# Optimization experiments

Hardware: AMD Instinct MI355X
Metric: run time of the kernel (lower is better)

Reference implementation:

```python
import jax, jax.numpy as jnp
import numpy as np

B, N1, N2, D, K = 8, 2048, 512, 128, 32
LEVELS, RES, BASE, FC = 3, 3, 0.25, 192
R3 = RES ** 3  # 27 voxel bins per level
EPS = 1e-5


def group_norm(x, gamma, beta, groups):
    # x: [b, C, ...]; normalize per (group) over channel-subset + spatial dims
    b, c = x.shape[0], x.shape[1]
    xg = x.reshape(b, groups, -1)
    mu = xg.mean(axis=-1, keepdims=True)
    var = xg.var(axis=-1, keepdims=True)
    xn = ((xg - mu) * jax.lax.rsqrt(var + EPS)).reshape(x.shape)
    shape = (1, c) + (1,) * (x.ndim - 2)
    return xn * gamma.reshape(shape) + beta.reshape(shape)


def prelu(x, a):
    return jnp.where(x >= 0, x, a * x)


def setup_inputs() -> dict:
    key = jax.random.key(0)
    ks = jax.random.split(key, 12)
    def w(k, shape):
        fan_in = shape[-1]
        return jax.random.uniform(k, shape, jnp.float32, -1.0, 1.0) / jnp.sqrt(jnp.float32(fan_in))
    return {
        "coords": jax.random.normal(ks[0], (B, N1, 3), jnp.float32),
        "coords2": jax.random.normal(ks[1], (B, N2, 3), jnp.float32),
        "fmap1": jax.random.normal(ks[2], (B, D, N1), jnp.float32),
        "fmap2": jax.random.normal(ks[3], (B, D, N2), jnp.float32),
        # vol_conv: Conv1d(81,128,1) -> GN(8,128) -> PReLU -> Conv1d(128,192,1)
        "W1": w(ks[4], (128, R3 * LEVELS)), "b1": jnp.zeros((128,), jnp.float32),
        "g1": jnp.ones((128,), jnp.float32), "be1": jnp.zeros((128,), jnp.float32),
        "a1": jnp.array(0.25, jnp.float32),
        "W2": w(ks[5], (FC, 128)), "b2": jnp.zeros((FC,), jnp.float32),
        # knn_conv: Conv2d(4,64,1) -> GN(8,64) -> PReLU;  knn_out: Conv1d(64,192,1)
        "Wk": w(ks[6], (64, 4)), "bk": jnp.zeros((64,), jnp.float32),
        "gk": jnp.ones((64,), jnp.float32), "bek": jnp.zeros((64,), jnp.float32),
        "ak": jnp.array(0.25, jnp.float32),
        "Wo": w(ks[7], (FC, 64)), "bo": jnp.zeros((FC,), jnp.float32),
    }


def reference(coords, coords2, fmap1, fmap2, W1, b1, g1, be1, a1, W2, b2,
              Wk, bk, gk, bek, ak, Wo, bo):
    b, n1 = coords.shape[0], coords.shape[1]
    n2 = coords2.shape[1]
    dim = fmap1.shape[1]

    # correlation: [b, n1, n2]
    corr = jnp.einsum('bdn,bdm->bnm', fmap1, fmap2) / jnp.sqrt(jnp.float32(dim))
    # pairwise offsets template - search: [b, n1, n2, 3]
    diff = coords2[:, None, :, :] - coords[:, :, None, :]

    # --- multi-level voxel feature via scatter-add ---
    base = jnp.arange(b * n1, dtype=jnp.int32).reshape(b, n1, 1) * R3
    feats = []
    for i in range(LEVELS):
        r = BASE * (2 ** i)
        dv = jnp.round(diff / r)
        valid = jnp.all(jnp.abs(dv) <= (RES // 2), axis=-1)          # [b,n1,n2]
        dvi = (dv + 1.0).astype(jnp.int32)
        cube = dvi[..., 0] * (RES * RES) + dvi[..., 1] * RES + dvi[..., 2]
        idx = jnp.where(valid, cube, 0)                              # torch: cube*valid
        seg = (base + idx).reshape(-1)
        vf = valid.astype(corr.dtype)
        nseg = b * n1 * R3
        add = jax.ops.segment_sum((corr * vf).reshape(-1), seg, num_segments=nseg).reshape(b, n1, R3)
        cnt = jax.ops.segment_sum(vf.reshape(-1), seg, num_segments=nseg).reshape(b, n1, R3)
        feats.append((add / jnp.clip(cnt, 1.0, float(n1))).transpose(0, 2, 1))  # [b,R3,n1]
    vol = jnp.concatenate(feats, axis=1)                             # [b, 3*27, n1]

    h = jnp.einsum('oc,bcn->bon', W1, vol) + b1[None, :, None]
    h = prelu(group_norm(h, g1, be1, 8), a1)
    vol_out = jnp.einsum('oc,bcn->bon', W2, h) + b2[None, :, None]   # [b, FC, n1]

    # --- KNN feature ---
    dist = jnp.sum(diff * diff, axis=-1)                             # [b,n1,n2]
    _, nbr = jax.lax.top_k(-dist, K)                                 # [b,n1,K]
    knn_corr = jnp.take_along_axis(corr, nbr, axis=2)                # [b,n1,K]
    knn_xyz = jnp.take_along_axis(diff, nbr[..., None], axis=2)      # [b,n1,K,3]
    e = jnp.concatenate([knn_corr[:, None], knn_xyz.transpose(0, 3, 1, 2)], axis=1)  # [b,4,n1,K]
    h = jnp.einsum('oc,bcnk->bonk', Wk, e) + bk[None, :, None, None]
    h = prelu(group_norm(h, gk, bek, 8), ak)
    h = jnp.max(h, axis=3)                                           # [b,64,n1]
    knn_out = jnp.einsum('oc,bcn->bon', Wo, h) + bo[None, :, None]   # [b,FC,n1]

    return vol_out + knn_out
```

## Files before the change

kernel.cpp:

```cpp
#include <hip/hip_runtime.h>
#include <hip/hip_bf16.h>

#define N1 2048
#define N2 512
#define KNN 32

typedef unsigned short u16;
typedef unsigned int u32;
typedef unsigned long long u64;
typedef __attribute__((ext_vector_type(8))) short bf16x8;
typedef __attribute__((ext_vector_type(4))) float f32x4;

#define OFF_W1B  18432
#define OFF_GV   36864
#define OFF_GK   36992
#define OFF_FLAG 37120
#define OFF_H1   37128
#define OFF_KM   1085704
#define OFF_CO   1609992

__device__ __forceinline__ float tof(u16 u) {
  union { u32 i; float f; } v; v.i = ((u32)u) << 16; return v.f;
}
__device__ __forceinline__ u16 tob(float f) {
  __hip_bfloat16 h = __float2bfloat16(f);
  return *reinterpret_cast<u16*>(&h);
}
__device__ __forceinline__ float fs(float v) {
  return (fabsf(v) < 1e30f) ? v : 0.f;
}

template <int BF>
__device__ __forceinline__ float LD(const void* p, size_t i) {
  if (BF) return tof(((const u16*)p)[i]);
  return ((const float*)p)[i];
}
template <int BF>
__device__ __forceinline__ void ST(void* p, size_t i, float v) {
  if (BF) ((u16*)p)[i] = tob(v);
  else    ((float*)p)[i] = v;
}

__device__ __forceinline__ u32 umin32(u32 a, u32 b) { return a < b ? a : b; }

__device__ __forceinline__ u32 wave_min_u32(u32 v) {
  v = umin32(v, (u32)__builtin_amdgcn_update_dpp((int)0xFFFFFFFF, (int)v, 0x111, 0xf, 0xf, false));
  v = umin32(v, (u32)__builtin_amdgcn_update_dpp((int)0xFFFFFFFF, (int)v, 0x112, 0xf, 0xf, false));
  v = umin32(v, (u32)__builtin_amdgcn_update_dpp((int)0xFFFFFFFF, (int)v, 0x114, 0xf, 0xf, false));
  v = umin32(v, (u32)__builtin_amdgcn_update_dpp((int)0xFFFFFFFF, (int)v, 0x118, 0xf, 0xf, false));
  v = umin32(v, (u32)__builtin_amdgcn_update_dpp((int)0xFFFFFFFF, (int)v, 0x142, 0xa, 0xf, false));
  v = umin32(v, (u32)__builtin_amdgcn_update_dpp((int)0xFFFFFFFF, (int)v, 0x143, 0xc, 0xf, false));
  return (u32)__builtin_amdgcn_readlane((int)v, 63);
}

template <int BF>
__device__ __forceinline__ bf16x8 ld_wfrag(const void* W2, const void* Wo,
                                           int o, int k0) {
  if (BF) {
    const u16* p = (k0 < 128) ? (const u16*)W2 + (size_t)o * 128 + k0
                              : (const u16*)Wo + (size_t)o * 64 + (k0 - 128);
    return *(const bf16x8*)p;
  } else {
    const float* p = (k0 < 128) ? (const float*)W2 + (size_t)o * 128 + k0
                                : (const float*)Wo + (size_t)o * 64 + (k0 - 128);
    bf16x8 r;
#pragma unroll
    for (int j = 0; j < 8; j++) r[j] = (short)tob(p[j]);
    return r;
  }
}

template <int BF>
__device__ void prep_body(const void* W1, float* ws, int i0, int stride) {
  u16* w1b = (u16*)(ws + OFF_W1B);
  for (int i = i0; i < 128 * 96; i += stride) {
    int c = i / 96, j = i % 96;
    float v = (j < 81) ? LD<BF>(W1, c * 81 + j) : 0.f;
    w1b[i] = tob(fs(v));
  }
}

__global__ __launch_bounds__(256) void k_prep(const void* fmap1, const void* W1,
                                              float* ws) {
  int t = threadIdx.x;
  __shared__ int sbad;
  if (t == 0) sbad = 0;
  __syncthreads();
  int bad = 0;
  const u16* fm = (const u16*)fmap1;
  for (int i = t * 8; i < t * 8 + 8; i++) {
    float v = tof(fm[i]);
    if (!(fabsf(v) <= 64.f)) bad = 1;
  }
  if (bad) atomicOr(&sbad, 1);
  __syncthreads();
  int bf = sbad ? 0 : 1;
  if (blockIdx.x == 0) {
    if (t == 0) ((int*)(ws + OFF_FLAG))[0] = bf;
    (ws + OFF_GV)[t] = 0.f;
  }
  int i0 = blockIdx.x * 256 + t, stride = gridDim.x * 256;
  if (bf) prep_body<1>(W1, ws, i0, stride);
  else    prep_body<0>(W1, ws, i0, stride);
}

template <int BF>
__device__ void corr_stage(const void* f1, const void* f2, u16* As, u16* Bs,
                           int b, int m0, int n0, int t) {
#pragma unroll
  for (int rep = 0; rep < 2; rep++) {
    int i = t + rep * 256;
    int m8 = i & 15, d4 = i >> 4;
    u16 e[4][8];
    if (BF) {
      const u16* F1 = (const u16*)f1;
#pragma unroll
      for (int dr = 0; dr < 4; dr++) {
        uint4 v = *(const uint4*)&F1[(size_t)(b * 128 + d4 * 4 + dr) * N1 + m0 + m8 * 8];
        u32 w[4] = {v.x, v.y, v.z, v.w};
#pragma unroll
        for (int j = 0; j < 8; j++) e[dr][j] = (u16)(w[j >> 1] >> ((j & 1) * 16));
      }
    } else {
      const float* F1 = (const float*)f1;
#pragma unroll
      for (int dr = 0; dr < 4; dr++) {
        const float* src = &F1[(size_t)(b * 128 + d4 * 4 + dr) * N1 + m0 + m8 * 8];
        float4 a = *(const float4*)src, c = *(const float4*)(src + 4);
        float f[8] = {a.x, a.y, a.z, a.w, c.x, c.y, c.z, c.w};
#pragma unroll
        for (int j = 0; j < 8; j++) e[dr][j] = tob(f[j]);
      }
    }
#pragma unroll
    for (int j = 0; j < 8; j++) {
      u64 pk = (u64)e[0][j] | ((u64)e[1][j] << 16) | ((u64)e[2][j] << 32) |
               ((u64)e[3][j] << 48);
      *(u64*)&As[(m8 * 8 + j) * 136 + d4 * 4] = pk;
    }
  }
  {
    int n8 = t & 7, d4 = t >> 3;
    u16 e[4][8];
    if (BF) {
      const u16* F2 = (const u16*)f2;
#pragma unroll
      for (int dr = 0; dr < 4; dr++) {
        uint4 v = *(const uint4*)&F2[(size_t)(b * 128 + d4 * 4 + dr) * N2 + n0 + n8 * 8];
        u32 w[4] = {v.x, v.y, v.z, v.w};
#pragma unroll
        for (int j = 0; j < 8; j++) e[dr][j] = (u16)(w[j >> 1] >> ((j & 1) * 16));
      }
    } else {
      const float* F2 = (const float*)f2;
#pragma unroll
      for (int dr = 0; dr < 4; dr++) {
        const float* src = &F2[(size_t)(b * 128 + d4 * 4 + dr) * N2 + n0 + n8 * 8];
        float4 a = *(const float4*)src, c = *(const float4*)(src + 4);
        float f[8] = {a.x, a.y, a.z, a.w, c.x, c.y, c.z, c.w};
#pragma unroll
        for (int j = 0; j < 8; j++) e[dr][j] = tob(f[j]);
      }
    }
#pragma unroll
    for (int j = 0; j < 8; j++) {
      u64 pk = (u64)e[0][j] | ((u64)e[1][j] << 16) | ((u64)e[2][j] << 32) |
               ((u64)e[3][j] << 48);
      *(u64*)&Bs[(n8 * 8 + j) * 136 + d4 * 4] = pk;
    }
  }
}

__global__ __launch_bounds__(256) void k_corr(const int* flag,
                                              const void* f1, const void* f2,
                                              u16* corrb) {
  __shared__ __attribute__((aligned(16))) u16 As[128 * 136];
  __shared__ __attribute__((aligned(16))) u16 Bs[64 * 136];
  int b = blockIdx.z, m0 = blockIdx.x * 128, n0 = blockIdx.y * 64, t = threadIdx.x;
  if (*flag) corr_stage<1>(f1, f2, As, Bs, b, m0, n0, t);
  else       corr_stage<0>(f1, f2, As, Bs, b, m0, n0, t);
  __syncthreads();

  int wv = t >> 6, lane = t & 63;
  int l15 = lane & 15, q = lane >> 4;
  int wm = (wv >> 1) * 64, wn = (wv & 1) * 32;
  f32x4 acc[4][2];
#pragma unroll
  for (int mt = 0; mt < 4; mt++)
#pragma unroll
    for (int nt = 0; nt < 2; nt++) acc[mt][nt] = (f32x4){0.f, 0.f, 0.f, 0.f};

#pragma unroll
  for (int kc = 0; kc < 128; kc += 32) {
    bf16x8 af[4], bf[2];
#pragma unroll
    for (int mt = 0; mt < 4; mt++)
      af[mt] = *(const bf16x8*)&As[(wm + mt * 16 + l15) * 136 + kc + q * 8];
#pragma unroll
    for (int nt = 0; nt < 2; nt++)
      bf[nt] = *(const bf16x8*)&Bs[(wn + nt * 16 + l15) * 136 + kc + q * 8];
#pragma unroll
    for (int mt = 0; mt < 4; mt++)
#pragma unroll
      for (int nt = 0; nt < 2; nt++)
        acc[mt][nt] = __builtin_amdgcn_mfma_f32_16x16x32_bf16(
            af[mt], bf[nt], acc[mt][nt], 0, 0, 0);
  }
  const float s = 0.08838834764831843f;
#pragma unroll
  for (int mt = 0; mt < 4; mt++)
#pragma unroll
    for (int nt = 0; nt < 2; nt++)
#pragma unroll
      for (int r = 0; r < 4; r++) {
        int m = m0 + wm + mt * 16 + q * 4 + r;
        int n = n0 + wn + nt * 16 + l15;
        corrb[((size_t)(b * N1 + m)) * N2 + n] = tob(acc[mt][nt][r] * s);
      }
}

template <int BF>
__device__ void pv_body(const void* coords, const void* coords2,
                        const u16* corrb, const void* Wk, const void* bk,
                        const u16* w1b, const void* b1,
                        u16* h1b, u16* knnmax,
                        float* gvolraw, float* gknnraw,
                        float* c2s, float* binsum, float* bincnt,
                        float4* e_s, u16* volb, float* statv, float* statk,
                        int b, int p0, int t) {
  int wv = t >> 6, lane = t & 63;
  int l15 = lane & 15, q = lane >> 4;
  for (int i = t; i < N2 * 3; i += 256) c2s[i] = LD<BF>(coords2, b * N2 * 3 + i);
  for (int i = t; i < 208; i += 256) ((uint4*)volb)[i] = make_uint4(0, 0, 0, 0);
  if (t < 16) { statv[t] = 0.f; statk[t] = 0.f; }
  __syncthreads();

  for (int s = 0; s < 2; s++) {
    int pp = wv * 2 + s;
    int p = p0 + pp;
    for (int i = lane; i < 81; i += 64) {
      binsum[wv * 81 + i] = 0.f;
      bincnt[wv * 81 + i] = 0.f;
    }
    float px = LD<BF>(coords, (b * N1 + p) * 3 + 0);
    float py = LD<BF>(coords, (b * N1 + p) * 3 + 1);
    float pz = LD<BF>(coords, (b * N1 + p) * 3 + 2);
    const u16* crow = corrb + ((size_t)(b * N1 + p)) * N2;

    u64 kk[8];
#pragma unroll
    for (int i = 0; i < 8; i++) {
      int n2 = i * 64 + lane;
      float cv = tof(crow[n2]);
      float dx = c2s[n2 * 3 + 0] - px;
      float dy = c2s[n2 * 3 + 1] - py;
      float dz = c2s[n2 * 3 + 2] - pz;
      float dist = __fadd_rn(__fadd_rn(__fmul_rn(dx, dx), __fmul_rn(dy, dy)),
                             __fmul_rn(dz, dz));
      union { float f; u32 u; } du; du.f = dist;
      kk[i] = (((u64)du.u) << 32) | (u64)n2;
      float sc = 4.f;
#pragma unroll
      for (int lvl = 0; lvl < 3; lvl++) {
        float vx = rintf(dx * sc), vy = rintf(dy * sc), vz = rintf(dz * sc);
        if (fabsf(vx) <= 1.f && fabsf(vy) <= 1.f && fabsf(vz) <= 1.f) {
          int cube = ((int)vx + 1) * 9 + ((int)vy + 1) * 3 + ((int)vz + 1);
          atomicAdd(&binsum[wv * 81 + lvl * 27 + cube], cv);
          atomicAdd(&bincnt[wv * 81 + lvl * 27 + cube], 1.f);
        }
        sc *= 0.5f;
      }
    }

#define CAS(a, b) { u64 x = kk[a], y = kk[b]; bool sw = y < x; \
                    kk[a] = sw ? y : x; kk[b] = sw ? x : y; }
    CAS(0,1) CAS(2,3) CAS(4,5) CAS(6,7)
    CAS(0,2) CAS(1,3) CAS(4,6) CAS(5,7)
    CAS(1,2) CAS(5,6)
    CAS(0,4) CAS(1,5) CAS(2,6) CAS(3,7)
    CAS(2,4) CAS(3,5)
    CAS(1,2) CAS(3,4) CAS(5,6)
#undef CAS
    int my_idx = 0;
    for (int it = 0; it < KNN; it++) {
      u32 hb = (u32)(kk[0] >> 32);
      u32 wb = wave_min_u32(hb);
      u64 mask = __ballot(hb == wb);
      u32 widx;
      if (__builtin_popcountll(mask) == 1) {
        int wl = (int)__builtin_ctzll(mask);
        widx = (u32)__builtin_amdgcn_readlane((int)(u32)kk[0], wl);
      } else {
        u32 hidx = (hb == wb) ? (u32)kk[0] : 0xFFFFFFFFu;
        widx = wave_min_u32(hidx);
      }
      if (lane == it) my_idx = (int)widx;
      if (lane == (int)(widx & 63u)) {
        kk[0] = kk[1]; kk[1] = kk[2]; kk[2] = kk[3]; kk[3] = kk[4];
        kk[4] = kk[5]; kk[5] = kk[6]; kk[6] = kk[7]; kk[7] = ~0ull;
      }
    }
    if (lane < KNN) {
      float4 ev;
      ev.x = tof(crow[my_idx]);
      ev.y = c2s[my_idx * 3 + 0] - px;
      ev.z = c2s[my_idx * 3 + 1] - py;
      ev.w = c2s[my_idx * 3 + 2] - pz;
      e_s[wv * 32 + lane] = ev;
    }
#pragma unroll
    for (int rep = 0; rep < 2; rep++) {
      int i = lane + rep * 64;
      if (i < 96) {
        float v = (i < 81)
            ? binsum[wv * 81 + i] / fmaxf(bincnt[wv * 81 + i], 1.f) : 0.f;
        volb[pp * 104 + i] = tob(v);
      }
    }

    {
      int cch = lane;
      float w0 = LD<BF>(Wk, cch * 4 + 0), w1 = LD<BF>(Wk, cch * 4 + 1);
      float w2 = LD<BF>(Wk, cch * 4 + 2), w3 = LD<BF>(Wk, cch * 4 + 3);
      float bv = LD<BF>(bk, cch);
      float sm = 0.f, sq = 0.f, mx = -3e38f;
#pragma unroll 8
      for (int k = 0; k < KNN; k++) {
        float4 ev = e_s[wv * 32 + k];
        float h = bv + w0 * ev.x + w1 * ev.y + w2 * ev.z + w3 * ev.w;
        sm += h; sq += h * h; mx = fmaxf(mx, h);
      }
      knnmax[((size_t)(b * N1 + p)) * 64 + cch] = tob(mx);
      sm += __shfl_xor(sm, 1, 64); sq += __shfl_xor(sq, 1, 64);
      sm += __shfl_xor(sm, 2, 64); sq += __shfl_xor(sq, 2, 64);
      sm += __shfl_xor(sm, 4, 64); sq += __shfl_xor(sq, 4, 64);
      if ((lane & 7) == 0) {
        int g = cch >> 3;
        atomicAdd(&statk[g * 2 + 0], sm);
        atomicAdd(&statk[g * 2 + 1], sq);
      }
    }
  }
  __syncthreads();

  f32x4 acc[2];
  acc[0] = (f32x4){0.f, 0.f, 0.f, 0.f};
  acc[1] = (f32x4){0.f, 0.f, 0.f, 0.f};
#pragma unroll
  for (int kc = 0; kc < 96; kc += 32) {
    bf16x8 af = *(const bf16x8*)&volb[l15 * 104 + kc + q * 8];
    bf16x8 bf0 = *(const bf16x8*)&w1b[((2 * wv + 0) * 16 + l15) * 96 + kc + q * 8];
    bf16x8 bf1 = *(const bf16x8*)&w1b[((2 * wv + 1) * 16 + l15) * 96 + kc + q * 8];
    acc[0] = __builtin_amdgcn_mfma_f32_16x16x32_bf16(af, bf0, acc[0], 0, 0, 0);
    acc[1] = __builtin_amdgcn_mfma_f32_16x16x32_bf16(af, bf1, acc[1], 0, 0, 0);
  }
#pragma unroll
  for (int ct = 0; ct < 2; ct++) {
    int c = (2 * wv + ct) * 16 + l15;
    float bias = LD<BF>(b1, c);
    float sm = 0.f, sq = 0.f;
    if (q < 2) {
#pragma unroll
      for (int r = 0; r < 4; r++) {
        int p = p0 + q * 4 + r;
        float v = acc[ct][r] + bias;
        h1b[((size_t)(b * N1 + p)) * 128 + c] = tob(v);
        sm += v; sq += v * v;
      }
    }
    sm += __shfl_xor(sm, 1, 64);  sq += __shfl_xor(sq, 1, 64);
    sm += __shfl_xor(sm, 2, 64);  sq += __shfl_xor(sq, 2, 64);
    sm += __shfl_xor(sm, 4, 64);  sq += __shfl_xor(sq, 4, 64);
    sm += __shfl_xor(sm, 8, 64);  sq += __shfl_xor(sq, 8, 64);
    sm += __shfl_xor(sm, 16, 64); sq += __shfl_xor(sq, 16, 64);
    sm += __shfl_xor(sm, 32, 64); sq += __shfl_xor(sq, 32, 64);
    if (lane == 0) {
      int g = 2 * wv + ct;
      atomicAdd(&statv[g * 2 + 0], sm);
      atomicAdd(&statv[g * 2 + 1], sq);
    }
  }
  __syncthreads();
  if (t < 16) atomicAdd(&gvolraw[b * 16 + t], statv[t]);
  else if (t < 32) atomicAdd(&gknnraw[b * 16 + (t - 16)], statk[t - 16]);
}

__global__ __launch_bounds__(256) void k_pv(const int* flag,
                                            const void* coords, const void* coords2,
                                            const u16* corrb, const void* Wk,
                                            const void* bk, const u16* w1b,
                                            const void* b1, u16* h1b,
                                            u16* knnmax, float* gvolraw,
                                            float* gknnraw) {
  __shared__ float c2s[N2 * 3];
  __shared__ float binsum[4 * 81];
  __shared__ float bincnt[4 * 81];
  __shared__ float4 e_s[4 * 32];
  __shared__ __attribute__((aligned(16))) u16 volb[16 * 104];
  __shared__ float statv[16], statk[16];
  int b = blockIdx.y, p0 = blockIdx.x * 8, t = threadIdx.x;
  if (*flag)
    pv_body<1>(coords, coords2, corrb, Wk, bk, w1b, b1, h1b, knnmax,
               gvolraw, gknnraw, c2s, binsum, bincnt, e_s, volb, statv, statk,
               b, p0, t);
  else
    pv_body<0>(coords, coords2, corrb, Wk, bk, w1b, b1, h1b, knnmax,
               gvolraw, gknnraw, c2s, binsum, bincnt, e_s, volb, statv, statk,
               b, p0, t);
}

template <int BF>
__device__ void out_body(const u16* h1b, const u16* knnmax,
                         const void* W2, const void* Wo,
                         const float* gvolraw, const float* gknnraw,
                         const void* g1, const void* be1, const void* a1p,
                         const void* gk, const void* bek, const void* akp,
                         const void* b2, const void* bo, void* out,
                         float* Ac, float* Bc, float* Sc, float* Bi, u16* gs,
                         int b, int p0, int t) {
  if (t < 192) {
    float A, Bv, slope;
    if (t < 128) {
      int g = t >> 4;
      float S = fs(gvolraw[b * 16 + g * 2 + 0]);
      float Q = fs(gvolraw[b * 16 + g * 2 + 1]);
      float mean = S / 32768.f;
      float var = fmaxf(Q / 32768.f - mean * mean, 0.f);
      float inv = 1.f / sqrtf(var + 1e-5f);
      A = inv * LD<BF>(g1, t); Bv = LD<BF>(be1, t) - mean * A;
      slope = LD<BF>(a1p, 0);
    } else {
      int c = t - 128, g = c >> 3;
      float S = fs(gknnraw[b * 16 + g * 2 + 0]);
      float Q = fs(gknnraw[b * 16 + g * 2 + 1]);
      float mean = S / 524288.f;
      float var = fmaxf(Q / 524288.f - mean * mean, 0.f);
      float inv = 1.f / sqrtf(var + 1e-5f);
      A = inv * LD<BF>(gk, c); Bv = LD<BF>(bek, c) - mean * A;
      slope = LD<BF>(akp, 0);
    }
    Ac[t] = A; Bc[t] = Bv; Sc[t] = slope;
    Bi[t] = LD<BF>(b2, t) + LD<BF>(bo, t);
  }
  __syncthreads();

  for (int i = t; i < 768; i += 256) {
    int p = i / 24, c8 = i % 24;
    int c0 = c8 * 8;
    uint4 v;
    if (c8 < 16) v = *(const uint4*)&h1b[((size_t)(b * N1 + p0 + p)) * 128 + c0];
    else         v = *(const uint4*)&knnmax[((size_t)(b * N1 + p0 + p)) * 64 + (c0 - 128)];
    u16 e[8] = {(u16)(v.x & 0xffff), (u16)(v.x >> 16), (u16)(v.y & 0xffff),
                (u16)(v.y >> 16),    (u16)(v.z & 0xffff), (u16)(v.z >> 16),
                (u16)(v.w & 0xffff), (u16)(v.w >> 16)};
    u16 r[8];
#pragma unroll
    for (int j = 0; j < 8; j++) {
      int c = c0 + j;
      float xn = tof(e[j]) * Ac[c] + Bc[c];
      xn = xn >= 0.f ? xn : Sc[c] * xn;
      r[j] = tob(xn);
    }
    uint4 wv;
    wv.x = (u32)r[0] | ((u32)r[1] << 16);
    wv.y = (u32)r[2] | ((u32)r[3] << 16);
    wv.z = (u32)r[4] | ((u32)r[5] << 16);
    wv.w = (u32)r[6] | ((u32)r[7] << 16);
    *(uint4*)&gs[p * 200 + c0] = wv;
  }
  __syncthreads();

  int wv2 = t >> 6, lane = t & 63;
  int l15 = lane & 15, q = lane >> 4;
  int obase = wv2 * 48;
  f32x4 acc[3][2];
#pragma unroll
  for (int mt = 0; mt < 3; mt++)
#pragma unroll
    for (int nt = 0; nt < 2; nt++) acc[mt][nt] = (f32x4){0.f, 0.f, 0.f, 0.f};

#pragma unroll
  for (int kc = 0; kc < 192; kc += 32) {
    bf16x8 af[3], bf[2];
#pragma unroll
    for (int mt = 0; mt < 3; mt++)
      af[mt] = ld_wfrag<BF>(W2, Wo, obase + mt * 16 + l15, kc + q * 8);
#pragma unroll
    for (int nt = 0; nt < 2; nt++)
      bf[nt] = *(const bf16x8*)&gs[(nt * 16 + l15) * 200 + kc + q * 8];
#pragma unroll
    for (int mt = 0; mt < 3; mt++)
#pragma unroll
      for (int nt = 0; nt < 2; nt++)
        acc[mt][nt] = __builtin_amdgcn_mfma_f32_16x16x32_bf16(
            af[mt], bf[nt], acc[mt][nt], 0, 0, 0);
  }
#pragma unroll
  for (int mt = 0; mt < 3; mt++)
#pragma unroll
    for (int nt = 0; nt < 2; nt++)
#pragma unroll
      for (int r = 0; r < 4; r++) {
        int o = obase + mt * 16 + q * 4 + r;
        int p = p0 + nt * 16 + l15;
        ST<BF>(out, ((size_t)(b * 192 + o)) * N1 + p, fs(acc[mt][nt][r] + Bi[o]));
      }
}

__global__ __launch_bounds__(256) void k_out(const int* flag,
                                             const u16* h1b, const u16* knnmax,
                                             const void* W2, const void* Wo,
                                             const float* gvolraw, const float* gknnraw,
                                             const void* g1, const void* be1,
                                             const void* a1p, const void* gk,
                                             const void* bek, const void* akp,
                                             const void* b2, const void* bo,
                                             void* out) {
  __shared__ float Ac[192], Bc[192], Sc[192], Bi[192];
  __shared__ __attribute__((aligned(16))) u16 gs[32 * 200];
  int b = blockIdx.y, p0 = blockIdx.x * 32, t = threadIdx.x;
  if (*flag)
    out_body<1>(h1b, knnmax, W2, Wo, gvolraw, gknnraw, g1, be1, a1p, gk, bek,
                akp, b2, bo, out, Ac, Bc, Sc, Bi, gs, b, p0, t);
  else
    out_body<0>(h1b, knnmax, W2, Wo, gvolraw, gknnraw, g1, be1, a1p, gk, bek,
                akp, b2, bo, out, Ac, Bc, Sc, Bi, gs, b, p0, t);
}

extern "C" void kernel_launch(void* const* d_in, const int* in_sizes, int n_in,
                              void* d_out, int out_size, void* d_ws, size_t ws_size,
                              hipStream_t stream) {
  const void* coords  = d_in[0];
  const void* coords2 = d_in[1];
  const void* fmap1   = d_in[2];
  const void* fmap2   = d_in[3];
  const void* W1  = d_in[4];
  const void* b1  = d_in[5];
  const void* g1  = d_in[6];
  const void* be1 = d_in[7];
  const void* a1  = d_in[8];
  const void* W2  = d_in[9];
  const void* b2  = d_in[10];
  const void* Wk  = d_in[11];
  const void* bk  = d_in[12];
  const void* gk  = d_in[13];
  const void* bek = d_in[14];
  const void* ak  = d_in[15];
  const void* Wo  = d_in[16];
  const void* bo  = d_in[17];

  float* ws = (float*)d_ws;
  u16* w1b       = (u16*)(ws + OFF_W1B);
  float* gvolraw = ws + OFF_GV;
  float* gknnraw = ws + OFF_GK;
  const int* flag = (const int*)(ws + OFF_FLAG);
  u16* h1b    = (u16*)(ws + OFF_H1);
  u16* knnmax = (u16*)(ws + OFF_KM);
  u16* corrb  = (u16*)(ws + OFF_CO);

  k_prep<<<dim3(8), dim3(256), 0, stream>>>(fmap1, W1, ws);
  k_corr<<<dim3(16, 8, 8), dim3(256), 0, stream>>>(flag, fmap1, fmap2, corrb);
  k_pv<<<dim3(256, 8), dim3(256), 0, stream>>>(flag, coords, coords2, corrb,
                                               Wk, bk, w1b, b1, h1b, knnmax,
                                               gvolraw, gknnraw);
  k_out<<<dim3(64, 8), dim3(256), 0, stream>>>(flag, h1b, knnmax, W2, Wo,
                                               gvolraw, gknnraw, g1, be1, a1,
                                               gk, bek, ak, b2, bo, d_out);
}
```

Baseline: 208.2 us.

## Fold prep kernel into corr, detect dtype per block, and pair-process KNN points per wave

Removes the separate prep kernel: every block now re-detects the input dtype from fmap1 itself, and one corr block converts W1 and zeroes the stats buffer. In k_pv each wave now handles its two points at once, interleaving the distance, binning, top-k selection and the fused DPP min reduction so both chains share latency. This drops one launch and adds ILP in the serial selection loop, at the cost of more registers and doubled shared bin buffers. It also relies on the corr block finishing the W1 conversion before k_pv reads it, which holds under stream ordering.

Result: slower. 214.6 us (+3.1%).

```diff
diff --git a/kernel.cpp b/kernel.cpp
--- a/kernel.cpp
+++ b/kernel.cpp
@@ -14,7 +14,6 @@
 #define OFF_W1B  18432
 #define OFF_GV   36864
 #define OFF_GK   36992
-#define OFF_FLAG 37120
 #define OFF_H1   37128
 #define OFF_KM   1085704
 #define OFF_CO   1609992
@@ -43,14 +42,33 @@
 
 __device__ __forceinline__ u32 umin32(u32 a, u32 b) { return a < b ? a : b; }
 
-__device__ __forceinline__ u32 wave_min_u32(u32 v) {
-  v = umin32(v, (u32)__builtin_amdgcn_update_dpp((int)0xFFFFFFFF, (int)v, 0x111, 0xf, 0xf, false));
-  v = umin32(v, (u32)__builtin_amdgcn_update_dpp((int)0xFFFFFFFF, (int)v, 0x112, 0xf, 0xf, false));
-  v = umin32(v, (u32)__builtin_amdgcn_update_dpp((int)0xFFFFFFFF, (int)v, 0x114, 0xf, 0xf, false));
-  v = umin32(v, (u32)__builtin_amdgcn_update_dpp((int)0xFFFFFFFF, (int)v, 0x118, 0xf, 0xf, false));
-  v = umin32(v, (u32)__builtin_amdgcn_update_dpp((int)0xFFFFFFFF, (int)v, 0x142, 0xa, 0xf, false));
-  v = umin32(v, (u32)__builtin_amdgcn_update_dpp((int)0xFFFFFFFF, (int)v, 0x143, 0xc, 0xf, false));
-  return (u32)__builtin_amdgcn_readlane((int)v, 63);
+__device__ __forceinline__ int detect_flag(const void* fmap1, int t, int* sbad) {
+  if (t == 0) *sbad = 0;
+  __syncthreads();
+  uint4 v = ((const uint4*)fmap1)[t];
+  u32 w[4] = {v.x, v.y, v.z, v.w};
+  int bad = 0;
+#pragma unroll
+  for (int j = 0; j < 8; j++) {
+    float f = tof((u16)(w[j >> 1] >> ((j & 1) * 16)));
+    if (!(fabsf(f) <= 64.f)) bad = 1;
+  }
+  if (bad) atomicOr(sbad, 1);
+  __syncthreads();
+  return *sbad ? 0 : 1;
+}
+
+__device__ __forceinline__ void wave_min2(u32& a, u32& b) {
+  u32 ta, tb;
+#define STEP(ctl, rm) \
+  ta = (u32)__builtin_amdgcn_update_dpp((int)0xFFFFFFFF, (int)a, ctl, rm, 0xf, false); \
+  tb = (u32)__builtin_amdgcn_update_dpp((int)0xFFFFFFFF, (int)b, ctl, rm, 0xf, false); \
+  a = umin32(a, ta); b = umin32(b, tb);
+  STEP(0x111, 0xf) STEP(0x112, 0xf) STEP(0x114, 0xf) STEP(0x118, 0xf)
+  STEP(0x142, 0xa) STEP(0x143, 0xc)
+#undef STEP
+  a = (u32)__builtin_amdgcn_readlane((int)a, 63);
+  b = (u32)__builtin_amdgcn_readlane((int)b, 63);
 }
 
 template <int BF>
@@ -71,42 +89,10 @@
 }
 
 template <int BF>
-__device__ void prep_body(const void* W1, float* ws, int i0, int stride) {
-  u16* w1b = (u16*)(ws + OFF_W1B);
-  for (int i = i0; i < 128 * 96; i += stride) {
-    int c = i / 96, j = i % 96;
-    float v = (j < 81) ? LD<BF>(W1, c * 81 + j) : 0.f;
-    w1b[i] = tob(fs(v));
-  }
-}
-
-__global__ __launch_bounds__(256) void k_prep(const void* fmap1, const void* W1,
-                                              float* ws) {
-  int t = threadIdx.x;
-  __shared__ int sbad;
-  if (t == 0) sbad = 0;
-  __syncthreads();
-  int bad = 0;
-  const u16* fm = (const u16*)fmap1;
-  for (int i = t * 8; i < t * 8 + 8; i++) {
-    float v = tof(fm[i]);
-    if (!(fabsf(v) <= 64.f)) bad = 1;
-  }
-  if (bad) atomicOr(&sbad, 1);
-  __syncthreads();
-  int bf = sbad ? 0 : 1;
-  if (blockIdx.x == 0) {
-    if (t == 0) ((int*)(ws + OFF_FLAG))[0] = bf;
-    (ws + OFF_GV)[t] = 0.f;
-  }
-  int i0 = blockIdx.x * 256 + t, stride = gridDim.x * 256;
-  if (bf) prep_body<1>(W1, ws, i0, stride);
-  else    prep_body<0>(W1, ws, i0, stride);
-}
-
-template <int BF>
-__device__ void corr_stage(const void* f1, const void* f2, u16* As, u16* Bs,
-                           int b, int m0, int n0, int t) {
+__device__ void corr_body(const void* f1, const void* f2, const void* W1,
+                          u16* w1b, float* stats, u16* corrb,
+                          u16* As, u16* Bs, int b, int m0, int n0, int t,
+                          int prep) {
 #pragma unroll
   for (int rep = 0; rep < 2; rep++) {
     int i = t + rep * 256;
@@ -169,16 +155,6 @@
       *(u64*)&Bs[(n8 * 8 + j) * 136 + d4 * 4] = pk;
     }
   }
-}
-
-__global__ __launch_bounds__(256) void k_corr(const int* flag,
-                                              const void* f1, const void* f2,
-                                              u16* corrb) {
-  __shared__ __attribute__((aligned(16))) u16 As[128 * 136];
-  __shared__ __attribute__((aligned(16))) u16 Bs[64 * 136];
-  int b = blockIdx.z, m0 = blockIdx.x * 128, n0 = blockIdx.y * 64, t = threadIdx.x;
-  if (*flag) corr_stage<1>(f1, f2, As, Bs, b, m0, n0, t);
-  else       corr_stage<0>(f1, f2, As, Bs, b, m0, n0, t);
   __syncthreads();
 
   int wv = t >> 6, lane = t & 63;
@@ -217,6 +193,30 @@
         int n = n0 + wn + nt * 16 + l15;
         corrb[((size_t)(b * N1 + m)) * N2 + n] = tob(acc[mt][nt][r] * s);
       }
+
+  if (prep) {
+    for (int i = t; i < 128 * 96; i += 256) {
+      int c = i / 96, j = i % 96;
+      float v = (j < 81) ? LD<BF>(W1, c * 81 + j) : 0.f;
+      w1b[i] = tob(fs(v));
+    }
+    stats[t] = 0.f;
+  }
+}
+
+__global__ __launch_bounds__(256) void k_corr(const void* f1, const void* f2,
+                                              const void* W1, float* ws,
+                                              u16* corrb) {
+  __shared__ __attribute__((aligned(16))) u16 As[128 * 136];
+  __shared__ __attribute__((aligned(16))) u16 Bs[64 * 136];
+  __shared__ int sbad;
+  int b = blockIdx.z, m0 = blockIdx.x * 128, n0 = blockIdx.y * 64, t = threadIdx.x;
+  int bf = detect_flag(f1, t, &sbad);
+  int prep = (blockIdx.x == 0 && blockIdx.y == 0 && blockIdx.z == 0);
+  u16* w1b = (u16*)(ws + OFF_W1B);
+  float* stats = ws + OFF_GV;
+  if (bf) corr_body<1>(f1, f2, W1, w1b, stats, corrb, As, Bs, b, m0, n0, t, prep);
+  else    corr_body<0>(f1, f2, W1, w1b, stats, corrb, As, Bs, b, m0, n0, t, prep);
 }
 
 template <int BF>
@@ -232,113 +232,148 @@
   int l15 = lane & 15, q = lane >> 4;
   for (int i = t; i < N2 * 3; i += 256) c2s[i] = LD<BF>(coords2, b * N2 * 3 + i);
   for (int i = t; i < 208; i += 256) ((uint4*)volb)[i] = make_uint4(0, 0, 0, 0);
+  for (int i = t; i < 648; i += 256) { binsum[i] = 0.f; bincnt[i] = 0.f; }
   if (t < 16) { statv[t] = 0.f; statk[t] = 0.f; }
   __syncthreads();
 
-  for (int s = 0; s < 2; s++) {
-    int pp = wv * 2 + s;
-    int p = p0 + pp;
-    for (int i = lane; i < 81; i += 64) {
-      binsum[wv * 81 + i] = 0.f;
-      bincnt[wv * 81 + i] = 0.f;
-    }
-    float px = LD<BF>(coords, (b * N1 + p) * 3 + 0);
-    float py = LD<BF>(coords, (b * N1 + p) * 3 + 1);
-    float pz = LD<BF>(coords, (b * N1 + p) * 3 + 2);
-    const u16* crow = corrb + ((size_t)(b * N1 + p)) * N2;
-
-    u64 kk[8];
-#pragma unroll
-    for (int i = 0; i < 8; i++) {
-      int n2 = i * 64 + lane;
-      float cv = tof(crow[n2]);
-      float dx = c2s[n2 * 3 + 0] - px;
-      float dy = c2s[n2 * 3 + 1] - py;
-      float dz = c2s[n2 * 3 + 2] - pz;
-      float dist = __fadd_rn(__fadd_rn(__fmul_rn(dx, dx), __fmul_rn(dy, dy)),
-                             __fmul_rn(dz, dz));
-      union { float f; u32 u; } du; du.f = dist;
-      kk[i] = (((u64)du.u) << 32) | (u64)n2;
-      float sc = 4.f;
-#pragma unroll
-      for (int lvl = 0; lvl < 3; lvl++) {
-        float vx = rintf(dx * sc), vy = rintf(dy * sc), vz = rintf(dz * sc);
-        if (fabsf(vx) <= 1.f && fabsf(vy) <= 1.f && fabsf(vz) <= 1.f) {
-          int cube = ((int)vx + 1) * 9 + ((int)vy + 1) * 3 + ((int)vz + 1);
-          atomicAdd(&binsum[wv * 81 + lvl * 27 + cube], cv);
-          atomicAdd(&bincnt[wv * 81 + lvl * 27 + cube], 1.f);
-        }
-        sc *= 0.5f;
-      }
-    }
-
-#define CAS(a, b) { u64 x = kk[a], y = kk[b]; bool sw = y < x; \
-                    kk[a] = sw ? y : x; kk[b] = sw ? x : y; }
-    CAS(0,1) CAS(2,3) CAS(4,5) CAS(6,7)
-    CAS(0,2) CAS(1,3) CAS(4,6) CAS(5,7)
-    CAS(1,2) CAS(5,6)
-    CAS(0,4) CAS(1,5) CAS(2,6) CAS(3,7)
-    CAS(2,4) CAS(3,5)
-    CAS(1,2) CAS(3,4) CAS(5,6)
-#undef CAS
-    int my_idx = 0;
-    for (int it = 0; it < KNN; it++) {
-      u32 hb = (u32)(kk[0] >> 32);
-      u32 wb = wave_min_u32(hb);
-      u64 mask = __ballot(hb == wb);
-      u32 widx;
-      if (__builtin_popcountll(mask) == 1) {
-        int wl = (int)__builtin_ctzll(mask);
-        widx = (u32)__builtin_amdgcn_readlane((int)(u32)kk[0], wl);
-      } else {
-        u32 hidx = (hb == wb) ? (u32)kk[0] : 0xFFFFFFFFu;
-        widx = wave_min_u32(hidx);
-      }
-      if (lane == it) my_idx = (int)widx;
-      if (lane == (int)(widx & 63u)) {
-        kk[0] = kk[1]; kk[1] = kk[2]; kk[2] = kk[3]; kk[3] = kk[4];
-        kk[4] = kk[5]; kk[5] = kk[6]; kk[6] = kk[7]; kk[7] = ~0ull;
-      }
-    }
-    if (lane < KNN) {
-      float4 ev;
-      ev.x = tof(crow[my_idx]);
-      ev.y = c2s[my_idx * 3 + 0] - px;
-      ev.z = c2s[my_idx * 3 + 1] - py;
-      ev.w = c2s[my_idx * 3 + 2] - pz;
-      e_s[wv * 32 + lane] = ev;
-    }
-#pragma unroll
-    for (int rep = 0; rep < 2; rep++) {
-      int i = lane + rep * 64;
-      if (i < 96) {
-        float v = (i < 81)
-            ? binsum[wv * 81 + i] / fmaxf(bincnt[wv * 81 + i], 1.f) : 0.f;
-        volb[pp * 104 + i] = tob(v);
-      }
-    }
-
-    {
-      int cch = lane;
-      float w0 = LD<BF>(Wk, cch * 4 + 0), w1 = LD<BF>(Wk, cch * 4 + 1);
-      float w2 = LD<BF>(Wk, cch * 4 + 2), w3 = LD<BF>(Wk, cch * 4 + 3);
-      float bv = LD<BF>(bk, cch);
-      float sm = 0.f, sq = 0.f, mx = -3e38f;
+  int ps0 = wv * 2, ps1 = ps0 + 1;
+  int pA = p0 + ps0, pB = p0 + ps1;
+  float px0 = LD<BF>(coords, (b * N1 + pA) * 3 + 0);
+  float py0 = LD<BF>(coords, (b * N1 + pA) * 3 + 1);
+  float pz0 = LD<BF>(coords, (b * N1 + pA) * 3 + 2);
+  float px1 = LD<BF>(coords, (b * N1 + pB) * 3 + 0);
+  float py1 = LD<BF>(coords, (b * N1 + pB) * 3 + 1);
+  float pz1 = LD<BF>(coords, (b * N1 + pB) * 3 + 2);
+  const u16* crow0 = corrb + ((size_t)(b * N1 + pA)) * N2;
+  const u16* crow1 = crow0 + N2;
+
+  u64 kk0[8], kk1[8];
+#pragma unroll
+  for (int i = 0; i < 8; i++) {
+    int n2 = i * 64 + lane;
+    float cv0 = tof(crow0[n2]);
+    float cv1 = tof(crow1[n2]);
+    float cx = c2s[n2 * 3 + 0], cy = c2s[n2 * 3 + 1], cz = c2s[n2 * 3 + 2];
+    float dx0 = cx - px0, dy0 = cy - py0, dz0 = cz - pz0;
+    float dx1 = cx - px1, dy1 = cy - py1, dz1 = cz - pz1;
+    float d0 = __fadd_rn(__fadd_rn(__fmul_rn(dx0, dx0), __fmul_rn(dy0, dy0)),
+                         __fmul_rn(dz0, dz0));
+    float d1 = __fadd_rn(__fadd_rn(__fmul_rn(dx1, dx1), __fmul_rn(dy1, dy1)),
+                         __fmul_rn(dz1, dz1));
+    union { float f; u32 u; } u0, u1;
+    u0.f = d0; u1.f = d1;
+    kk0[i] = (((u64)u0.u) << 32) | (u64)n2;
+    kk1[i] = (((u64)u1.u) << 32) | (u64)n2;
+    float sc = 4.f;
+#pragma unroll
+    for (int lvl = 0; lvl < 3; lvl++) {
+      float vx0 = rintf(dx0 * sc), vy0 = rintf(dy0 * sc), vz0 = rintf(dz0 * sc);
+      float vx1 = rintf(dx1 * sc), vy1 = rintf(dy1 * sc), vz1 = rintf(dz1 * sc);
+      if (fabsf(vx0) <= 1.f && fabsf(vy0) <= 1.f && fabsf(vz0) <= 1.f) {
+        int cube = ((int)vx0 + 1) * 9 + ((int)vy0 + 1) * 3 + ((int)vz0 + 1);
+        atomicAdd(&binsum[ps0 * 81 + lvl * 27 + cube], cv0);
+        atomicAdd(&bincnt[ps0 * 81 + lvl * 27 + cube], 1.f);
+      }
+      if (fabsf(vx1) <= 1.f && fabsf(vy1) <= 1.f && fabsf(vz1) <= 1.f) {
+        int cube = ((int)vx1 + 1) * 9 + ((int)vy1 + 1) * 3 + ((int)vz1 + 1);
+        atomicAdd(&binsum[ps1 * 81 + lvl * 27 + cube], cv1);
+        atomicAdd(&bincnt[ps1 * 81 + lvl * 27 + cube], 1.f);
+      }
+      sc *= 0.5f;
+    }
+  }
+
+#define CAS2(a, b) { u64 x = kk0[a], y = kk0[b]; bool sw = y < x;          \
+                     kk0[a] = sw ? y : x; kk0[b] = sw ? x : y;             \
+                     u64 x1 = kk1[a], y1 = kk1[b]; bool s1 = y1 < x1;      \
+                     kk1[a] = s1 ? y1 : x1; kk1[b] = s1 ? x1 : y1; }
+  CAS2(0,1) CAS2(2,3) CAS2(4,5) CAS2(6,7)
+  CAS2(0,2) CAS2(1,3) CAS2(4,6) CAS2(5,7)
+  CAS2(1,2) CAS2(5,6)
+  CAS2(0,4) CAS2(1,5) CAS2(2,6) CAS2(3,7)
+  CAS2(2,4) CAS2(3,5)
+  CAS2(1,2) CAS2(3,4) CAS2(5,6)
+#undef CAS2
+  int my_idx0 = 0, my_idx1 = 0;
+  for (int it = 0; it < KNN; it++) {
+    u32 hb0 = (u32)(kk0[0] >> 32);
+    u32 hb1 = (u32)(kk1[0] >> 32);
+    u32 wb0 = hb0, wb1 = hb1;
+    wave_min2(wb0, wb1);
+    u64 m0 = __ballot(hb0 == wb0);
+    u64 m1 = __ballot(hb1 == wb1);
+    u32 widx0, widx1;
+    if (__builtin_popcountll(m0) == 1 && __builtin_popcountll(m1) == 1) {
+      widx0 = (u32)__builtin_amdgcn_readlane((int)(u32)kk0[0],
+                                             (int)__builtin_ctzll(m0));
+      widx1 = (u32)__builtin_amdgcn_readlane((int)(u32)kk1[0],
+                                             (int)__builtin_ctzll(m1));
+    } else {
+      u32 h0 = (hb0 == wb0) ? (u32)kk0[0] : 0xFFFFFFFFu;
+      u32 h1 = (hb1 == wb1) ? (u32)kk1[0] : 0xFFFFFFFFu;
+      wave_min2(h0, h1);
+      widx0 = h0; widx1 = h1;
+    }
+    if (lane == it) { my_idx0 = (int)widx0; my_idx1 = (int)widx1; }
+    if (lane == (int)(widx0 & 63u)) {
+      kk0[0] = kk0[1]; kk0[1] = kk0[2]; kk0[2] = kk0[3]; kk0[3] = kk0[4];
+      kk0[4] = kk0[5]; kk0[5] = kk0[6]; kk0[6] = kk0[7]; kk0[7] = ~0ull;
+    }
+    if (lane == (int)(widx1 & 63u)) {
+      kk1[0] = kk1[1]; kk1[1] = kk1[2]; kk1[2] = kk1[3]; kk1[3] = kk1[4];
+      kk1[4] = kk1[5]; kk1[5] = kk1[6]; kk1[6] = kk1[7]; kk1[7] = ~0ull;
+    }
+  }
+  if (lane < KNN) {
+    float4 e0, e1;
+    e0.x = tof(crow0[my_idx0]);
+    e0.y = c2s[my_idx0 * 3 + 0] - px0;
+    e0.z = c2s[my_idx0 * 3 + 1] - py0;
+    e0.w = c2s[my_idx0 * 3 + 2] - pz0;
+    e1.x = tof(crow1[my_idx1]);
+    e1.y = c2s[my_idx1 * 3 + 0] - px1;
+    e1.z = c2s[my_idx1 * 3 + 1] - py1;
+    e1.w = c2s[my_idx1 * 3 + 2] - pz1;
+    e_s[ps0 * 32 + lane] = e0;
+    e_s[ps1 * 32 + lane] = e1;
+  }
+#pragma unroll
+  for (int rep = 0; rep < 2; rep++) {
+    int i = lane + rep * 64;
+    if (i < 96) {
+      float v0 = (i < 81)
+          ? binsum[ps0 * 81 + i] / fmaxf(bincnt[ps0 * 81 + i], 1.f) : 0.f;
+      float v1 = (i < 81)
+          ? binsum[ps1 * 81 + i] / fmaxf(bincnt[ps1 * 81 + i], 1.f) : 0.f;
+      volb[ps0 * 104 + i] = tob(v0);
+      volb[ps1 * 104 + i] = tob(v1);
+    }
+  }
+
+  {
+    int cch = lane;
+    float w0 = LD<BF>(Wk, cch * 4 + 0), w1 = LD<BF>(Wk, cch * 4 + 1);
+    float w2 = LD<BF>(Wk, cch * 4 + 2), w3 = LD<BF>(Wk, cch * 4 + 3);
+    float bv = LD<BF>(bk, cch);
+    float sm = 0.f, sq = 0.f, mx0 = -3e38f, mx1 = -3e38f;
 #pragma unroll 8
-      for (int k = 0; k < KNN; k++) {
-        float4 ev = e_s[wv * 32 + k];
-        float h = bv + w0 * ev.x + w1 * ev.y + w2 * ev.z + w3 * ev.w;
-        sm += h; sq += h * h; mx = fmaxf(mx, h);
-      }
-      knnmax[((size_t)(b * N1 + p)) * 64 + cch] = tob(mx);
-      sm += __shfl_xor(sm, 1, 64); sq += __shfl_xor(sq, 1, 64);
-      sm += __shfl_xor(sm, 2, 64); sq += __shfl_xor(sq, 2, 64);
-      sm += __shfl_xor(sm, 4, 64); sq += __shfl_xor(sq, 4, 64);
-      if ((lane & 7) == 0) {
-        int g = cch >> 3;
-        atomicAdd(&statk[g * 2 + 0], sm);
-        atomicAdd(&statk[g * 2 + 1], sq);
-      }
+    for (int k = 0; k < KNN; k++) {
+      float4 e0 = e_s[ps0 * 32 + k];
+      float4 e1 = e_s[ps1 * 32 + k];
+      float h0 = bv + w0 * e0.x + w1 * e0.y + w2 * e0.z + w3 * e0.w;
+      float h1 = bv + w0 * e1.x + w1 * e1.y + w2 * e1.z + w3 * e1.w;
+      sm += h0 + h1; sq += h0 * h0 + h1 * h1;
+      mx0 = fmaxf(mx0, h0); mx1 = fmaxf(mx1, h1);
+    }
+    knnmax[((size_t)(b * N1 + pA)) * 64 + cch] = tob(mx0);
+    knnmax[((size_t)(b * N1 + pB)) * 64 + cch] = tob(mx1);
+    sm += __shfl_xor(sm, 1, 64); sq += __shfl_xor(sq, 1, 64);
+    sm += __shfl_xor(sm, 2, 64); sq += __shfl_xor(sq, 2, 64);
+    sm += __shfl_xor(sm, 4, 64); sq += __shfl_xor(sq, 4, 64);
+    if ((lane & 7) == 0) {
+      int g = cch >> 3;
+      atomicAdd(&statk[g * 2 + 0], sm);
+      atomicAdd(&statk[g * 2 + 1], sq);
     }
   }
   __syncthreads();
@@ -385,21 +420,23 @@
   else if (t < 32) atomicAdd(&gknnraw[b * 16 + (t - 16)], statk[t - 16]);
 }
 
-__global__ __launch_bounds__(256) void k_pv(const int* flag,
-                                            const void* coords, const void* coords2,
+__global__ __launch_bounds__(256) void k_pv(const void* coords, const void* coords2,
+                                            const void* fmap1,
                                             const u16* corrb, const void* Wk,
                                             const void* bk, const u16* w1b,
                                             const void* b1, u16* h1b,
                                             u16* knnmax, float* gvolraw,
                                             float* gknnraw) {
   __shared__ float c2s[N2 * 3];
-  __shared__ float binsum[4 * 81];
-  __shared__ float bincnt[4 * 81];
-  __shared__ float4 e_s[4 * 32];
+  __shared__ float binsum[8 * 81];
+  __shared__ float bincnt[8 * 81];
+  __shared__ float4 e_s[8 * 32];
   __shared__ __attribute__((aligned(16))) u16 volb[16 * 104];
   __shared__ float statv[16], statk[16];
+  __shared__ int sbad;
   int b = blockIdx.y, p0 = blockIdx.x * 8, t = threadIdx.x;
-  if (*flag)
+  int bf = detect_flag(fmap1, t, &sbad);
+  if (bf)
     pv_body<1>(coords, coords2, corrb, Wk, bk, w1b, b1, h1b, knnmax,
                gvolraw, gknnraw, c2s, binsum, bincnt, e_s, volb, statv, statk,
                b, p0, t);
@@ -507,7 +544,7 @@
       }
 }
 
-__global__ __launch_bounds__(256) void k_out(const int* flag,
+__global__ __launch_bounds__(256) void k_out(const void* fmap1,
                                              const u16* h1b, const u16* knnmax,
                                              const void* W2, const void* Wo,
                                              const float* gvolraw, const float* gknnraw,
@@ -518,8 +555,10 @@
                                              void* out) {
   __shared__ float Ac[192], Bc[192], Sc[192], Bi[192];
   __shared__ __attribute__((aligned(16))) u16 gs[32 * 200];
+  __shared__ int sbad;
   int b = blockIdx.y, p0 = blockIdx.x * 32, t = threadIdx.x;
-  if (*flag)
+  int bf = detect_flag(fmap1, t, &sbad);
+  if (bf)
     out_body<1>(h1b, knnmax, W2, Wo, gvolraw, gknnraw, g1, be1, a1p, gk, bek,
                 akp, b2, bo, out, Ac, Bc, Sc, Bi, gs, b, p0, t);
   else
@@ -553,17 +592,15 @@
   u16* w1b       = (u16*)(ws + OFF_W1B);
   float* gvolraw = ws + OFF_GV;
   float* gknnraw = ws + OFF_GK;
-  const int* flag = (const int*)(ws + OFF_FLAG);
   u16* h1b    = (u16*)(ws + OFF_H1);
   u16* knnmax = (u16*)(ws + OFF_KM);
   u16* corrb  = (u16*)(ws + OFF_CO);
 
-  k_prep<<<dim3(8), dim3(256), 0, stream>>>(fmap1, W1, ws);
-  k_corr<<<dim3(16, 8, 8), dim3(256), 0, stream>>>(flag, fmap1, fmap2, corrb);
-  k_pv<<<dim3(256, 8), dim3(256), 0, stream>>>(flag, coords, coords2, corrb,
+  k_corr<<<dim3(16, 8, 8), dim3(256), 0, stream>>>(fmap1, fmap2, W1, ws, corrb);
+  k_pv<<<dim3(256, 8), dim3(256), 0, stream>>>(coords, coords2, fmap1, corrb,
                                                Wk, bk, w1b, b1, h1b, knnmax,
                                                gvolraw, gknnraw);
-  k_out<<<dim3(64, 8), dim3(256), 0, stream>>>(flag, h1b, knnmax, W2, Wo,
+  k_out<<<dim3(64, 8), dim3(256), 0, stream>>>(fmap1, h1b, knnmax, W2, Wo,
                                                gvolraw, gknnraw, g1, be1, a1,
                                                gk, bek, ak, b2, bo, d_out);
 }
```

## Fold prep kernel into correlation kernel and shrink corr/out tiles

Applied to the files above, without the earlier changes.

Removes the separate k_prep launch. Each correlation block now re-runs the dtype check on the first fmap1 chunk, and block (0,0,0) also does the W1 conversion, stat zeroing and flag write. The correlation tile shrinks from 128x64 to 64x64 and the output-projection tile from 32 to 16 points, doubling both grids to raise parallelism. In exchange, every correlation block repeats the dtype check, and the smaller tiles reuse loaded operands less.

Result: slower. 215.0 us (+3.2%).

```diff
diff --git a/kernel.cpp b/kernel.cpp
--- a/kernel.cpp
+++ b/kernel.cpp
@@ -71,46 +71,12 @@
 }
 
 template <int BF>
-__device__ void prep_body(const void* W1, float* ws, int i0, int stride) {
-  u16* w1b = (u16*)(ws + OFF_W1B);
-  for (int i = i0; i < 128 * 96; i += stride) {
-    int c = i / 96, j = i % 96;
-    float v = (j < 81) ? LD<BF>(W1, c * 81 + j) : 0.f;
-    w1b[i] = tob(fs(v));
-  }
-}
-
-__global__ __launch_bounds__(256) void k_prep(const void* fmap1, const void* W1,
-                                              float* ws) {
-  int t = threadIdx.x;
-  __shared__ int sbad;
-  if (t == 0) sbad = 0;
-  __syncthreads();
-  int bad = 0;
-  const u16* fm = (const u16*)fmap1;
-  for (int i = t * 8; i < t * 8 + 8; i++) {
-    float v = tof(fm[i]);
-    if (!(fabsf(v) <= 64.f)) bad = 1;
-  }
-  if (bad) atomicOr(&sbad, 1);
-  __syncthreads();
-  int bf = sbad ? 0 : 1;
-  if (blockIdx.x == 0) {
-    if (t == 0) ((int*)(ws + OFF_FLAG))[0] = bf;
-    (ws + OFF_GV)[t] = 0.f;
-  }
-  int i0 = blockIdx.x * 256 + t, stride = gridDim.x * 256;
-  if (bf) prep_body<1>(W1, ws, i0, stride);
-  else    prep_body<0>(W1, ws, i0, stride);
-}
-
-template <int BF>
-__device__ void corr_stage(const void* f1, const void* f2, u16* As, u16* Bs,
-                           int b, int m0, int n0, int t) {
-#pragma unroll
-  for (int rep = 0; rep < 2; rep++) {
-    int i = t + rep * 256;
-    int m8 = i & 15, d4 = i >> 4;
+__device__ void corr_body(const void* f1, const void* f2, const void* W1,
+                          u16* w1b, float* stats, int* flag, u16* corrb,
+                          u16* As, u16* Bs, int b, int m0, int n0, int t,
+                          int prep, int bf) {
+  {
+    int m8 = t & 7, d4 = t >> 3;
     u16 e[4][8];
     if (BF) {
       const u16* F1 = (const u16*)f1;
@@ -169,54 +135,75 @@
       *(u64*)&Bs[(n8 * 8 + j) * 136 + d4 * 4] = pk;
     }
   }
-}
-
-__global__ __launch_bounds__(256) void k_corr(const int* flag,
-                                              const void* f1, const void* f2,
-                                              u16* corrb) {
-  __shared__ __attribute__((aligned(16))) u16 As[128 * 136];
-  __shared__ __attribute__((aligned(16))) u16 Bs[64 * 136];
-  int b = blockIdx.z, m0 = blockIdx.x * 128, n0 = blockIdx.y * 64, t = threadIdx.x;
-  if (*flag) corr_stage<1>(f1, f2, As, Bs, b, m0, n0, t);
-  else       corr_stage<0>(f1, f2, As, Bs, b, m0, n0, t);
   __syncthreads();
 
   int wv = t >> 6, lane = t & 63;
   int l15 = lane & 15, q = lane >> 4;
-  int wm = (wv >> 1) * 64, wn = (wv & 1) * 32;
-  f32x4 acc[4][2];
-#pragma unroll
-  for (int mt = 0; mt < 4; mt++)
-#pragma unroll
-    for (int nt = 0; nt < 2; nt++) acc[mt][nt] = (f32x4){0.f, 0.f, 0.f, 0.f};
+  int wm = wv * 16;
+  f32x4 acc[4];
+#pragma unroll
+  for (int nt = 0; nt < 4; nt++) acc[nt] = (f32x4){0.f, 0.f, 0.f, 0.f};
 
 #pragma unroll
   for (int kc = 0; kc < 128; kc += 32) {
-    bf16x8 af[4], bf[2];
-#pragma unroll
-    for (int mt = 0; mt < 4; mt++)
-      af[mt] = *(const bf16x8*)&As[(wm + mt * 16 + l15) * 136 + kc + q * 8];
-#pragma unroll
-    for (int nt = 0; nt < 2; nt++)
-      bf[nt] = *(const bf16x8*)&Bs[(wn + nt * 16 + l15) * 136 + kc + q * 8];
-#pragma unroll
-    for (int mt = 0; mt < 4; mt++)
-#pragma unroll
-      for (int nt = 0; nt < 2; nt++)
-        acc[mt][nt] = __builtin_amdgcn_mfma_f32_16x16x32_bf16(
-            af[mt], bf[nt], acc[mt][nt], 0, 0, 0);
+    bf16x8 af = *(const bf16x8*)&As[(wm + l15) * 136 + kc + q * 8];
+    bf16x8 bf4[4];
+#pragma unroll
+    for (int nt = 0; nt < 4; nt++)
+      bf4[nt] = *(const bf16x8*)&Bs[(nt * 16 + l15) * 136 + kc + q * 8];
+#pragma unroll
+    for (int nt = 0; nt < 4; nt++)
+      acc[nt] = __builtin_amdgcn_mfma_f32_16x16x32_bf16(af, bf4[nt], acc[nt], 0, 0, 0);
   }
   const float s = 0.08838834764831843f;
 #pragma unroll
-  for (int mt = 0; mt < 4; mt++)
-#pragma unroll
-    for (int nt = 0; nt < 2; nt++)
-#pragma unroll
-      for (int r = 0; r < 4; r++) {
-        int m = m0 + wm + mt * 16 + q * 4 + r;
-        int n = n0 + wn + nt * 16 + l15;
-        corrb[((size_t)(b * N1 + m)) * N2 + n] = tob(acc[mt][nt][r] * s);
-      }
+  for (int nt = 0; nt < 4; nt++)
+#pragma unroll
+    for (int r = 0; r < 4; r++) {
+      int m = m0 + wm + q * 4 + r;
+      int n = n0 + nt * 16 + l15;
+      corrb[((size_t)(b * N1 + m)) * N2 + n] = tob(acc[nt][r] * s);
+    }
+
+  if (prep) {
+    for (int i = t; i < 128 * 96; i += 256) {
+      int c = i / 96, j = i % 96;
+      float v = (j < 81) ? LD<BF>(W1, c * 81 + j) : 0.f;
+      w1b[i] = tob(fs(v));
+    }
+    stats[t] = 0.f;
+    if (t == 0) *flag = bf;
+  }
+}
+
+__global__ __launch_bounds__(256) void k_corr(const void* f1, const void* f2,
+                                              const void* W1, float* ws,
+                                              u16* corrb) {
+  __shared__ __attribute__((aligned(16))) u16 As[64 * 136];
+  __shared__ __attribute__((aligned(16))) u16 Bs[64 * 136];
+  __shared__ int sbad;
+  int b = blockIdx.z, m0 = blockIdx.x * 64, n0 = blockIdx.y * 64, t = threadIdx.x;
+  if (t == 0) sbad = 0;
+  __syncthreads();
+  {
+    uint4 v = ((const uint4*)f1)[t];
+    u32 w[4] = {v.x, v.y, v.z, v.w};
+    int bad = 0;
+#pragma unroll
+    for (int j = 0; j < 8; j++) {
+      float f = tof((u16)(w[j >> 1] >> ((j & 1) * 16)));
+      if (!(fabsf(f) <= 64.f)) bad = 1;
+    }
+    if (bad) atomicOr(&sbad, 1);
+  }
+  __syncthreads();
+  int bf = sbad ? 0 : 1;
+  int prep = (blockIdx.x == 0 && blockIdx.y == 0 && blockIdx.z == 0);
+  u16* w1b = (u16*)(ws + OFF_W1B);
+  float* stats = ws + OFF_GV;
+  int* flag = (int*)(ws + OFF_FLAG);
+  if (bf) corr_body<1>(f1, f2, W1, w1b, stats, flag, corrb, As, Bs, b, m0, n0, t, prep, bf);
+  else    corr_body<0>(f1, f2, W1, w1b, stats, flag, corrb, As, Bs, b, m0, n0, t, prep, bf);
 }
 
 template <int BF>
@@ -444,7 +431,7 @@
   }
   __syncthreads();
 
-  for (int i = t; i < 768; i += 256) {
+  for (int i = t; i < 384; i += 256) {
     int p = i / 24, c8 = i % 24;
     int c0 = c8 * 8;
     uint4 v;
@@ -473,38 +460,29 @@
   int wv2 = t >> 6, lane = t & 63;
   int l15 = lane & 15, q = lane >> 4;
   int obase = wv2 * 48;
-  f32x4 acc[3][2];
-#pragma unroll
-  for (int mt = 0; mt < 3; mt++)
-#pragma unroll
-    for (int nt = 0; nt < 2; nt++) acc[mt][nt] = (f32x4){0.f, 0.f, 0.f, 0.f};
+  f32x4 acc[3];
+#pragma unroll
+  for (int mt = 0; mt < 3; mt++) acc[mt] = (f32x4){0.f, 0.f, 0.f, 0.f};
 
 #pragma unroll
   for (int kc = 0; kc < 192; kc += 32) {
-    bf16x8 af[3], bf[2];
+    bf16x8 af[3];
 #pragma unroll
     for (int mt = 0; mt < 3; mt++)
       af[mt] = ld_wfrag<BF>(W2, Wo, obase + mt * 16 + l15, kc + q * 8);
-#pragma unroll
-    for (int nt = 0; nt < 2; nt++)
-      bf[nt] = *(const bf16x8*)&gs[(nt * 16 + l15) * 200 + kc + q * 8];
+    bf16x8 bf = *(const bf16x8*)&gs[l15 * 200 + kc + q * 8];
 #pragma unroll
     for (int mt = 0; mt < 3; mt++)
-#pragma unroll
-      for (int nt = 0; nt < 2; nt++)
-        acc[mt][nt] = __builtin_amdgcn_mfma_f32_16x16x32_bf16(
-            af[mt], bf[nt], acc[mt][nt], 0, 0, 0);
+      acc[mt] = __builtin_amdgcn_mfma_f32_16x16x32_bf16(af[mt], bf, acc[mt], 0, 0, 0);
   }
 #pragma unroll
   for (int mt = 0; mt < 3; mt++)
 #pragma unroll
-    for (int nt = 0; nt < 2; nt++)
-#pragma unroll
-      for (int r = 0; r < 4; r++) {
-        int o = obase + mt * 16 + q * 4 + r;
-        int p = p0 + nt * 16 + l15;
-        ST<BF>(out, ((size_t)(b * 192 + o)) * N1 + p, fs(acc[mt][nt][r] + Bi[o]));
-      }
+    for (int r = 0; r < 4; r++) {
+      int o = obase + mt * 16 + q * 4 + r;
+      int p = p0 + l15;
+      ST<BF>(out, ((size_t)(b * 192 + o)) * N1 + p, fs(acc[mt][r] + Bi[o]));
+    }
 }
 
 __global__ __launch_bounds__(256) void k_out(const int* flag,
@@ -517,8 +495,8 @@
                                              const void* b2, const void* bo,
                                              void* out) {
   __shared__ float Ac[192], Bc[192], Sc[192], Bi[192];
-  __shared__ __attribute__((aligned(16))) u16 gs[32 * 200];
-  int b = blockIdx.y, p0 = blockIdx.x * 32, t = threadIdx.x;
+  __shared__ __attribute__((aligned(16))) u16 gs[16 * 200];
+  int b = blockIdx.y, p0 = blockIdx.x * 16, t = threadIdx.x;
   if (*flag)
     out_body<1>(h1b, knnmax, W2, Wo, gvolraw, gknnraw, g1, be1, a1p, gk, bek,
                 akp, b2, bo, out, Ac, Bc, Sc, Bi, gs, b, p0, t);
@@ -558,12 +536,11 @@
   u16* knnmax = (u16*)(ws + OFF_KM);
   u16* corrb  = (u16*)(ws + OFF_CO);
 
-  k_prep<<<dim3(8), dim3(256), 0, stream>>>(fmap1, W1, ws);
-  k_corr<<<dim3(16, 8, 8), dim3(256), 0, stream>>>(flag, fmap1, fmap2, corrb);
+  k_corr<<<dim3(32, 8, 8), dim3(256), 0, stream>>>(fmap1, fmap2, W1, ws, corrb);
   k_pv<<<dim3(256, 8), dim3(256), 0, stream>>>(flag, coords, coords2, corrb,
                                                Wk, bk, w1b, b1, h1b, knnmax,
                                                gvolraw, gknnraw);
-  k_out<<<dim3(64, 8), dim3(256), 0, stream>>>(flag, h1b, knnmax, W2, Wo,
-                                               gvolraw, gknnraw, g1, be1, a1,
-                                               gk, bek, ak, b2, bo, d_out);
-}
+  k_out<<<dim3(128, 8), dim3(256), 0, stream>>>(flag, h1b, knnmax, W2, Wo,
+                                                gvolraw, gknnraw, g1, be1, a1,
+                                                gk, bek, ak, b2, bo, d_out);
+}
```
